# Kernel tuning notes

Hardware: AMD Instinct MI355X
Metric: run time of the kernel (lower is better)

The kernel has to match this reference:

```python
import jax, jax.numpy as jnp
import numpy as np

B, T, C = 2, 2048, 1024
H, DH = 16, 64          # n_heads = d_model // 64
WIN = 256               # sliding window size
K = 32                  # n_oscillators
DFF = 4096              # d_ff_hidden
NEG = -1e9


def setup_inputs() -> dict:
    key = jax.random.key(0)
    ks = jax.random.split(key, 16)
    sC = 1.0 / np.sqrt(C)
    sF = 1.0 / np.sqrt(DFF)
    sK = 1.0 / np.sqrt(K)
    return {
        "x": jax.random.normal(ks[0], (B, T, C), jnp.float32),
        "norm1_w": jnp.ones((C,), jnp.float32),
        "qkv_w": jax.random.normal(ks[1], (3 * C, C), jnp.float32) * sC,
        "qkv_b": jnp.zeros((3 * C,), jnp.float32),
        "proj_w": jax.random.normal(ks[2], (C, C), jnp.float32) * sC,
        "proj_b": jnp.zeros((C,), jnp.float32),
        "gate_w": jax.random.normal(ks[3], (1, C), jnp.float32) * 0.01,
        "gate_b": jnp.zeros((1,), jnp.float32),
        "trn_win": jax.random.normal(ks[4], (K, C), jnp.float32) * sC,
        "trn_wout": jax.random.normal(ks[5], (C, K), jnp.float32) * sK,
        "trn_gate_w": jax.random.normal(ks[6], (K, C), jnp.float32) * sC,
        "trn_gate_b": jnp.zeros((K,), jnp.float32),
        "trn_a_logit": jax.random.normal(ks[7], (K,), jnp.float32),
        "trn_theta": jax.random.uniform(ks[8], (K,), jnp.float32, 0.0, np.pi),
        "trn_res_scale": jnp.asarray(0.1, jnp.float32),
        "norm2_w": jnp.ones((C,), jnp.float32),
        "ffn_gate_w": jax.random.normal(ks[9], (DFF, C), jnp.float32) * sC,
        "ffn_up_w": jax.random.normal(ks[10], (DFF, C), jnp.float32) * sC,
        "ffn_down_w": jax.random.normal(ks[11], (C, DFF), jnp.float32) * sF,
    }


def _rms(z, w, eps=1e-6):
    return z * jax.lax.rsqrt(jnp.mean(z * z, axis=-1, keepdims=True) + eps) * w


def reference(x, norm1_w, qkv_w, qkv_b, proj_w, proj_b, gate_w, gate_b,
              trn_win, trn_wout, trn_gate_w, trn_gate_b, trn_a_logit,
              trn_theta, trn_res_scale, norm2_w, ffn_gate_w, ffn_up_w,
              ffn_down_w):
    h = _rms(x, norm1_w)

    # ---- windowed causal attention (dense mask, as in the original) ----
    qkv = h @ qkv_w.T + qkv_b                       # [B,T,3C]
    q, k, v = jnp.split(qkv, 3, axis=-1)
    heads = lambda t: t.reshape(B, T, H, DH).transpose(0, 2, 1, 3)  # [B,H,T,DH]
    q, k, v = heads(q), heads(k), heads(v)
    row = jnp.arange(T)[:, None]
    col = jnp.arange(T)[None, :]
    mask = jnp.where((col <= row) & (col >= row - WIN + 1), 0.0, NEG).astype(x.dtype)
    scores = jnp.einsum('bhqd,bhkd->bhqk', q, k) / jnp.sqrt(jnp.asarray(DH, x.dtype))
    attn = jax.nn.softmax(scores + mask, axis=-1)
    ao = jnp.einsum('bhqk,bhkd->bhqd', attn, v).transpose(0, 2, 1, 3).reshape(B, T, C)
    ao = ao @ proj_w.T + proj_b

    # ---- temporal resonance branch: K damped rotating oscillators ----
    u = h @ trn_win.T                               # [B,T,K] drive
    a = jax.nn.sigmoid(trn_a_logit)                 # amplitude in (0,1) (amplitude_max=1)
    ct, st = jnp.cos(trn_theta), jnp.sin(trn_theta)

    def step(carry, ut):
        sr, si = carry
        nsr = a * (ct * sr - st * si) + ut
        nsi = a * (st * sr + ct * si)
        return (nsr, nsi), nsr

    init = (jnp.zeros((B, K), x.dtype), jnp.zeros((B, K), x.dtype))
    _, ys = jax.lax.scan(step, init, u.transpose(1, 0, 2))  # ys: [T,B,K]
    y = ys.transpose(1, 0, 2)                                # [B,T,K]
    tg = jax.nn.sigmoid(h @ trn_gate_w.T + trn_gate_b)
    trn_out = ((tg * y) @ trn_wout.T) * trn_res_scale        # [B,T,C]

    # ---- sigmoid gate mix + residual ----
    g = jax.nn.sigmoid(h @ gate_w.T + gate_b)       # [B,T,1]
    x = x + g * ao + (1.0 - g) * trn_out

    # ---- SwiGLU FFN ----
    h2 = _rms(x, norm2_w)
    ffn = (jax.nn.silu(h2 @ ffn_gate_w.T) * (h2 @ ffn_up_w.T)) @ ffn_down_w.T
    return x + ffn
```

## Files before the change

kernel.cpp:

```cpp
#include <hip/hip_runtime.h>


typedef unsigned short u16;
typedef unsigned short u16x8 __attribute__((ext_vector_type(8)));
typedef __bf16 bf16x8 __attribute__((ext_vector_type(8)));
typedef float f32x4 __attribute__((ext_vector_type(4)));

#define DI static __device__ __forceinline__

DI u16 f2b(float f){
  union { float f; unsigned u; } v; v.f = f;
  unsigned r = v.u + 0x7FFFu + ((v.u >> 16) & 1u);
  return (u16)(r >> 16);
}
DI float b2f(u16 b){
  union { unsigned u; float f; } v; v.u = ((unsigned)b) << 16; return v.f;
}
DI u16x8 ld8(const u16* p){ return *(const u16x8*)p; }

DI f32x4 MFMA16(u16x8 a, u16x8 b, f32x4 c){
  return __builtin_amdgcn_mfma_f32_16x16x32_bf16(
      __builtin_bit_cast(bf16x8, a), __builtin_bit_cast(bf16x8, b), c, 0, 0, 0);
}

DI void async16(const void* g, void* l){
  void* gg = const_cast<void*>(g);
  __builtin_amdgcn_global_load_lds(
      (__attribute__((address_space(1))) void*)gg,
      (__attribute__((address_space(3))) void*)l, 16, 0, 0);
}

__global__ __launch_bounds__(256) void convert_w(
    const float* __restrict__ qkvw, const float* __restrict__ projw,
    const float* __restrict__ fgw, const float* __restrict__ fuw,
    const float* __restrict__ fdw, const float* __restrict__ twin,
    const float* __restrict__ tgw, const float* __restrict__ twout,
    u16* __restrict__ dst)
{
  size_t i = (size_t)blockIdx.x * 256 + threadIdx.x;
  if (i >= 4260352u) return;
  size_t e = i * 4;
  float4 v;
  if (e < 3145728u)        v = *(const float4*)(qkvw + e);
  else if (e < 4194304u)   v = *(const float4*)(projw + (e - 3145728u));
  else if (e < 12582912u){
    size_t i2 = e - 4194304u;
    int row = (int)(i2 >> 10), c = (int)(i2 & 1023);
    const float* src = (row & 1) ? fuw : fgw;
    v = *(const float4*)(src + (size_t)(row >> 1) * 1024 + c);
  }
  else if (e < 16777216u)  v = *(const float4*)(fdw + (e - 12582912u));
  else if (e < 16908288u){
    size_t i2 = e - 16777216u;
    int row = (int)(i2 >> 10), c = (int)(i2 & 1023);
    if (row < 32)      v = *(const float4*)(twin + row * 1024 + c);
    else if (row < 64) v = *(const float4*)(tgw + (row - 32) * 1024 + c);
    else               v = make_float4(0.f, 0.f, 0.f, 0.f);
  } else {
    v = *(const float4*)(twout + (e - 16908288u));
  }
  uint2 p;
  p.x = (unsigned)f2b(v.x) | ((unsigned)f2b(v.y) << 16);
  p.y = (unsigned)f2b(v.z) | ((unsigned)f2b(v.w) << 16);
  *(uint2*)(dst + e) = p;
}

__global__ __launch_bounds__(256) void zero_f32(float* __restrict__ p, int n4)
{
  int i = blockIdx.x * 256 + threadIdx.x;
  if (i < n4) ((float4*)p)[i] = make_float4(0.f, 0.f, 0.f, 0.f);
}

__global__ __launch_bounds__(256) void copy_f32(
    const float* __restrict__ src, float* __restrict__ dst)
{
  int i = blockIdx.x * 256 + threadIdx.x;
  ((float4*)dst)[i] = ((const float4*)src)[i];
}

__global__ __launch_bounds__(256) void rmsnorm_gate(
    const float* __restrict__ x, const float* __restrict__ w,
    const float* __restrict__ gw, const float* __restrict__ gb,
    u16* __restrict__ h, float* __restrict__ g)
{
  const int row = blockIdx.x, tid = threadIdx.x;
  const int wave = tid >> 6, lane = tid & 63;
  __shared__ float sb[8];
  float4 xv = ((const float4*)(x + (size_t)row * 1024))[tid];
  float ss = xv.x*xv.x + xv.y*xv.y + xv.z*xv.z + xv.w*xv.w;
#pragma unroll
  for (int m = 32; m; m >>= 1) ss += __shfl_xor(ss, m);
  if (lane == 0) sb[wave] = ss;
  __syncthreads();
  float rstd = rsqrtf((sb[0]+sb[1]+sb[2]+sb[3]) * (1.f/1024.f) + 1e-6f);
  float4 wv = ((const float4*)w)[tid];
  float h0 = xv.x*rstd*wv.x, h1 = xv.y*rstd*wv.y;
  float h2v = xv.z*rstd*wv.z, h3 = xv.w*rstd*wv.w;
  uint2 pk;
  pk.x = (unsigned)f2b(h0) | ((unsigned)f2b(h1) << 16);
  pk.y = (unsigned)f2b(h2v) | ((unsigned)f2b(h3) << 16);
  ((uint2*)(h + (size_t)row * 1024))[tid] = pk;
  float4 gv = ((const float4*)gw)[tid];
  float gd = h0*gv.x + h1*gv.y + h2v*gv.z + h3*gv.w;
#pragma unroll
  for (int m = 32; m; m >>= 1) gd += __shfl_xor(gd, m);
  if (lane == 0) sb[4 + wave] = gd;
  __syncthreads();
  if (tid == 0) g[row] = 1.f / (1.f + __expf(-(sb[4]+sb[5]+sb[6]+sb[7] + gb[0])));
}

__global__ __launch_bounds__(256) void rmsnorm_plain(
    const float* __restrict__ x, const float* __restrict__ w, u16* __restrict__ h)
{
  const int row = blockIdx.x, tid = threadIdx.x;
  const int wave = tid >> 6, lane = tid & 63;
  __shared__ float sb[4];
  float4 xv = ((const float4*)(x + (size_t)row * 1024))[tid];
  float ss = xv.x*xv.x + xv.y*xv.y + xv.z*xv.z + xv.w*xv.w;
#pragma unroll
  for (int m = 32; m; m >>= 1) ss += __shfl_xor(ss, m);
  if (lane == 0) sb[wave] = ss;
  __syncthreads();
  float rstd = rsqrtf((sb[0]+sb[1]+sb[2]+sb[3]) * (1.f/1024.f) + 1e-6f);
  float4 wv = ((const float4*)w)[tid];
  uint2 pk;
  pk.x = (unsigned)f2b(xv.x*rstd*wv.x) | ((unsigned)f2b(xv.y*rstd*wv.y) << 16);
  pk.y = (unsigned)f2b(xv.z*rstd*wv.z) | ((unsigned)f2b(xv.w*rstd*wv.w) << 16);
  ((uint2*)(h + (size_t)row * 1024))[tid] = pk;
}

template<int MODE>
__global__ __launch_bounds__(256) void gemm_bt(
    const u16* __restrict__ A, const u16* __restrict__ B,
    float* __restrict__ outF, float* __restrict__ outF2, u16* __restrict__ outB,
    const float* __restrict__ bias, const u16* __restrict__ aux16,
    const float* __restrict__ auxF, const float* __restrict__ auxG,
    int M, int N, int K)
{
  (void)M;
  __shared__ __align__(16) u16 sA[128 * 32];
  __shared__ __align__(16) u16 sB[128 * 32];
  const int tid = threadIdx.x;
  const int wave = tid >> 6, lane = tid & 63;
  const int lr = lane & 15, lq = lane >> 4;
  const int m0 = blockIdx.x * 128, n0 = blockIdx.y * 128;
  const int wm = (wave & 1) * 64, wn = (wave >> 1) * 64;
  const int ks = K / (int)gridDim.z;
  const int kbeg = (int)blockIdx.z * ks, kend = kbeg + ks;
  f32x4 acc[4][4] = {};
  const int srow = wave * 16 + (lane >> 2);
  const int scol = (lane & 3) * 8;
  const u16* gA = A + (size_t)(m0 + srow) * K + scol;
  const u16* gB = B + (size_t)(n0 + srow) * K + scol;
  u16* lA0 = &sA[(wave * 16) * 32];
  u16* lA1 = &sA[(64 + wave * 16) * 32];
  u16* lB0 = &sB[(wave * 16) * 32];
  u16* lB1 = &sB[(64 + wave * 16) * 32];
  const size_t K64 = (size_t)64 * K;

  for (int k0 = kbeg; k0 < kend; k0 += 32){
    async16(gA + k0,       lA0);
    async16(gA + K64 + k0, lA1);
    async16(gB + k0,       lB0);
    async16(gB + K64 + k0, lB1);
    __syncthreads();
    u16x8 af[4], bf[4];
#pragma unroll
    for (int i = 0; i < 4; i++) af[i] = ld8(&sA[(wm + i*16 + lr)*32 + lq*8]);
#pragma unroll
    for (int i = 0; i < 4; i++) bf[i] = ld8(&sB[(wn + i*16 + lr)*32 + lq*8]);
#pragma unroll
    for (int mi = 0; mi < 4; mi++)
#pragma unroll
      for (int ni = 0; ni < 4; ni++)
        acc[mi][ni] = MFMA16(af[mi], bf[ni], acc[mi][ni]);
    __syncthreads();
  }

  float scale6 = 0.f;
  if (MODE == 6) scale6 = auxF[0];

#pragma unroll
  for (int mi = 0; mi < 4; mi++){
    const int row = m0 + wm + mi*16 + lq*4;
#pragma unroll
    for (int ni = 0; ni < 4; ni++){
      const int col = n0 + wn + ni*16 + lr;
#pragma unroll
      for (int r = 0; r < 4; r++){
        const int rr = row + r;
        float v = acc[mi][ni][r];
        if (MODE == 0){
          outB[(size_t)rr * N + col] = f2b(v + bias[col]);
        } else if (MODE == 3){
          atomicAdd(&outF[(size_t)rr * N + col], v);
        } else if (MODE == 4){
          const size_t idx = (size_t)rr * N + col;
          float gg = auxG[rr];
          outF[idx] = auxF[idx] + gg * (v + bias[col]) + (1.f - gg) * b2f(aux16[idx]);
        } else if (MODE == 5){
          int bb = rr >> 11, tt = rr & 2047;
          if (col < 32) atomicAdd(&outF[((size_t)bb * 32 + col) * 2048 + tt], v);
          else if (col < 64) atomicAdd(&outF2[(size_t)rr * 32 + (col - 32)], v);
        } else if (MODE == 6){
          outB[(size_t)rr * N + col] = f2b(v * scale6);
        } else if (MODE == 7){
          float p = __shfl_xor(v, 1);
          float gval = (lr & 1) ? p : v;
          float uval = (lr & 1) ? v : p;
          float rv = gval / (1.f + __expf(-gval)) * uval;
          if (!(lr & 1))
            outB[(size_t)rr * (N >> 1) + (col >> 1)] = f2b(rv);
        }
      }
    }
  }
}

__global__ __launch_bounds__(256) void attn_win(
    const u16* __restrict__ qkv, u16* __restrict__ ao)
{
  const int blk = blockIdx.x;
  const int tile = blk & 31, hh = (blk >> 5) & 15, b = blk >> 9;
  const int t0 = tile * 64;
  const int tid = threadIdx.x, wave = tid >> 6, lane = tid & 63;
  const int lr = lane & 15, lq = lane >> 4;
  const int qt = t0 + wave * 16;
  __shared__ __align__(16) u16 sVt[64 * 40];
  __shared__ __align__(16) u16 sP[4][16 * 32];

  const u16* base = qkv + (size_t)b * 2048 * 3072 + hh * 64;
  const u16* qrow = base + (size_t)(qt + lr) * 3072 + lq * 8;
  u16x8 qf0 = ld8(qrow), qf1 = ld8(qrow + 32);
  const u16* kbase = base + 1024;
  const u16* vbase = base + 2048;

  f32x4 o0 = {0,0,0,0}, o1 = {0,0,0,0}, o2 = {0,0,0,0}, o3 = {0,0,0,0};
  float mrun[4] = {-1e30f, -1e30f, -1e30f, -1e30f};
  float lrun[4] = {0.f, 0.f, 0.f, 0.f};
  const float c1 = 0.125f * 1.44269504088896f;

  const int kb = (t0 >= 256) ? (t0 - 256) : 0;
  const int ntl = (t0 + 64 - kb) >> 5;
  for (int it = 0; it < ntl; ++it){
    const int kt = kb + it * 32;
    __syncthreads();
    if (tid < 128){
      const int key = tid & 31, dh = tid >> 5;
      const u16* gv = vbase + (size_t)(kt + key) * 3072 + dh * 16;
      u16x8 v0 = ld8(gv), v1 = ld8(gv + 8);
#pragma unroll
      for (int j = 0; j < 8; j++){
        sVt[(dh*16 + j)     * 40 + key] = v0[j];
        sVt[(dh*16 + 8 + j) * 40 + key] = v1[j];
      }
    }
    __syncthreads();
    const bool active = (kt < qt + 16) && (kt + 286 >= qt);
    if (!active) continue;

    f32x4 s0 = {0,0,0,0}, s1 = {0,0,0,0};
    {
      const u16* kr = kbase + (size_t)(kt + lr) * 3072 + lq * 8;
      u16x8 k00 = ld8(kr), k01 = ld8(kr + 32);
      const u16* kr1 = kr + (size_t)16 * 3072;
      u16x8 k10 = ld8(kr1), k11 = ld8(kr1 + 32);
      s0 = MFMA16(qf0, k00, s0); s0 = MFMA16(qf1, k01, s0);
      s1 = MFMA16(qf0, k10, s1); s1 = MFMA16(qf1, k11, s1);
    }
    float al[4];
#pragma unroll
    for (int r = 0; r < 4; r++){
      const int q = qt + lq * 4 + r;
      const int ca = kt + lr, cb = kt + 16 + lr;
      float a0 = (ca <= q && ca + 255 >= q) ? s0[r] : -1e30f;
      float a1 = (cb <= q && cb + 255 >= q) ? s1[r] : -1e30f;
      float mx = fmaxf(a0, a1);
      mx = fmaxf(mx, __shfl_xor(mx, 1));
      mx = fmaxf(mx, __shfl_xor(mx, 2));
      mx = fmaxf(mx, __shfl_xor(mx, 4));
      mx = fmaxf(mx, __shfl_xor(mx, 8));
      float mn = fmaxf(mrun[r], mx);
      al[r] = exp2f((mrun[r] - mn) * c1);
      mrun[r] = mn;
      float p0 = (a0 > -1e29f) ? exp2f((a0 - mn) * c1) : 0.f;
      float p1 = (a1 > -1e29f) ? exp2f((a1 - mn) * c1) : 0.f;
      float sm = p0 + p1;
      sm += __shfl_xor(sm, 1); sm += __shfl_xor(sm, 2);
      sm += __shfl_xor(sm, 4); sm += __shfl_xor(sm, 8);
      lrun[r] = lrun[r] * al[r] + sm;
      sP[wave][(lq*4 + r) * 32 + lr]      = f2b(p0);
      sP[wave][(lq*4 + r) * 32 + 16 + lr] = f2b(p1);
    }
#pragma unroll
    for (int r = 0; r < 4; r++){
      o0[r] *= al[r]; o1[r] *= al[r]; o2[r] *= al[r]; o3[r] *= al[r];
    }
    __builtin_amdgcn_s_waitcnt(0xc07f);
    u16x8 pf = ld8(&sP[wave][lr * 32 + lq * 8]);
    o0 = MFMA16(pf, ld8(&sVt[(lr)      * 40 + lq * 8]), o0);
    o1 = MFMA16(pf, ld8(&sVt[(16 + lr) * 40 + lq * 8]), o1);
    o2 = MFMA16(pf, ld8(&sVt[(32 + lr) * 40 + lq * 8]), o2);
    o3 = MFMA16(pf, ld8(&sVt[(48 + lr) * 40 + lq * 8]), o3);
  }

  u16* aor = ao + (size_t)(b * 2048 + qt + lq * 4) * 1024 + hh * 64 + lr;
#pragma unroll
  for (int r = 0; r < 4; r++){
    float inv = 1.f / lrun[r];
    u16* p = aor + (size_t)r * 1024;
    p[0]  = f2b(o0[r] * inv);
    p[16] = f2b(o1[r] * inv);
    p[32] = f2b(o2[r] * inv);
    p[48] = f2b(o3[r] * inv);
  }
}

__global__ __launch_bounds__(256) void scan_k(
    const float* __restrict__ u_t, const float* __restrict__ tgl,
    const float* __restrict__ tgb,
    const float* __restrict__ alog, const float* __restrict__ theta,
    u16* __restrict__ z)
{
  const int bk = blockIdx.x;
  const int b = bk >> 5, k = bk & 31;
  const int j = threadIdx.x;
  const float a = 1.f / (1.f + __expf(-alog[k]));
  const float th = theta[k];
  const float bk_bias = tgb[k];
  const float wr = a * __cosf(th), wi = a * __sinf(th);
  const float* ubp = u_t + ((size_t)b * 32 + k) * 2048 + j * 8;
  float4 ua = ((const float4*)ubp)[0];
  float4 ub4 = ((const float4*)ubp)[1];
  float ur[8] = {ua.x, ua.y, ua.z, ua.w, ub4.x, ub4.y, ub4.z, ub4.w};
  float sr = 0.f, si = 0.f;
#pragma unroll
  for (int i = 0; i < 8; i++){
    float nr = wr*sr - wi*si + ur[i];
    float ni = wi*sr + wr*si;
    sr = nr; si = ni;
  }
  float w2r = wr*wr - wi*wi, w2i = 2.f*wr*wi;
  float w4r = w2r*w2r - w2i*w2i, w4i = 2.f*w2r*w2i;
  float Ar = w4r*w4r - w4i*w4i, Ai = 2.f*w4r*w4i;
  __shared__ float4 sc[256];
  float4 cur; cur.x = Ar; cur.y = Ai; cur.z = sr; cur.w = si;
  sc[j] = cur;
  __syncthreads();
  for (int s = 1; s < 256; s <<= 1){
    float4 pv;
    const bool has = (j >= s);
    if (has) pv = sc[j - s];
    __syncthreads();
    if (has){
      float nar = cur.x*pv.x - cur.y*pv.y;
      float nai = cur.x*pv.y + cur.y*pv.x;
      float nbr = cur.x*pv.z - cur.y*pv.w + cur.z;
      float nbi = cur.x*pv.w + cur.y*pv.z + cur.w;
      cur.x = nar; cur.y = nai; cur.z = nbr; cur.w = nbi;
    }
    sc[j] = cur;
    __syncthreads();
  }
  float s_r = 0.f, s_i = 0.f;
  if (j > 0){ float4 pr = sc[j - 1]; s_r = pr.z; s_i = pr.w; }
  const float* tgp = tgl + ((size_t)b * 2048 + j * 8) * 32 + k;
  u16* zp = z + ((size_t)b * 2048 + j * 8) * 32 + k;
#pragma unroll
  for (int i = 0; i < 8; i++){
    float nr = wr*s_r - wi*s_i + ur[i];
    float ni = wi*s_r + wr*s_i;
    s_r = nr; s_i = ni;
    float tgv = 1.f / (1.f + __expf(-(tgp[(size_t)i * 32] + bk_bias)));
    zp[(size_t)i * 32] = f2b(s_r * tgv);
  }
}

extern "C" void kernel_launch(void* const* d_in, const int* in_sizes, int n_in,
                              void* d_out, int out_size, void* d_ws, size_t ws_size,
                              hipStream_t stream)
{
  (void)in_sizes; (void)n_in; (void)out_size; (void)ws_size;
  const float* x      = (const float*)d_in[0];
  const float* n1w    = (const float*)d_in[1];
  const float* qkvw   = (const float*)d_in[2];
  const float* qkvb   = (const float*)d_in[3];
  const float* projw  = (const float*)d_in[4];
  const float* projb  = (const float*)d_in[5];
  const float* gatew  = (const float*)d_in[6];
  const float* gateb  = (const float*)d_in[7];
  const float* twin   = (const float*)d_in[8];
  const float* twout  = (const float*)d_in[9];
  const float* tgw    = (const float*)d_in[10];
  const float* tgb    = (const float*)d_in[11];
  const float* talog  = (const float*)d_in[12];
  const float* ttheta = (const float*)d_in[13];
  const float* tscale = (const float*)d_in[14];
  const float* n2w    = (const float*)d_in[15];
  const float* fgw    = (const float*)d_in[16];
  const float* fuw    = (const float*)d_in[17];
  const float* fdw    = (const float*)d_in[18];
  float* out = (float*)d_out;

  char* wsb = (char*)d_ws;
  size_t off = 0;
  auto take = [&](size_t bytes) -> void* {
    void* r = wsb + off; off += (bytes + 255) & ~(size_t)255; return r;
  };
  u16*   wall = (u16*)take(17041408ull * 2);
  u16*   h    = (u16*)take(4194304ull * 2);
  u16*   h2   = (u16*)take(4194304ull * 2);
  u16*   trn  = (u16*)take(4194304ull * 2);
  float* g    = (float*)take(4096ull * 4);
  float* xmid = (float*)take(4194304ull * 4);
  float* uacc = (float*)take(262144ull * 4);
  float* tgl  = uacc + 131072;
  u16*   zz   = (u16*)take(131072ull * 2);
  u16*   regA = (u16*)take(4096ull * 4096 * 2);
  u16*   regB = (u16*)take(4096ull * 4096 * 2);

  u16* wq  = wall;
  u16* wp  = wall + 3145728;
  u16* wgu = wall + 4194304;
  u16* wd  = wall + 12582912;
  u16* wct = wall + 16777216;
  u16* wo  = wall + 16908288;
  u16* qkv = regA;
  u16* act = regA;
  u16* ao  = regB;

  convert_w<<<16642, 256, 0, stream>>>(qkvw, projw, fgw, fuw, fdw, twin, tgw, twout, wall);
  rmsnorm_gate<<<4096, 256, 0, stream>>>(x, n1w, gatew, gateb, h, g);
  zero_f32<<<256, 256, 0, stream>>>(uacc, 65536);
  gemm_bt<5><<<dim3(32, 1, 8), 256, 0, stream>>>(h, wct, uacc, tgl, nullptr, nullptr,
                                                 nullptr, nullptr, nullptr, 4096, 128, 1024);
  scan_k<<<64, 256, 0, stream>>>(uacc, tgl, tgb, talog, ttheta, zz);
  gemm_bt<6><<<dim3(32, 8), 256, 0, stream>>>(zz, wo, nullptr, nullptr, trn, nullptr,
                                              nullptr, tscale, nullptr, 4096, 1024, 32);
  gemm_bt<0><<<dim3(32, 24), 256, 0, stream>>>(h, wq, nullptr, nullptr, qkv, qkvb,
                                               nullptr, nullptr, nullptr, 4096, 3072, 1024);
  attn_win<<<1024, 256, 0, stream>>>(qkv, ao);
  gemm_bt<4><<<dim3(32, 8), 256, 0, stream>>>(ao, wp, xmid, nullptr, nullptr, projb,
                                              trn, x, g, 4096, 1024, 1024);
  rmsnorm_plain<<<4096, 256, 0, stream>>>(xmid, n2w, h2);
  gemm_bt<7><<<dim3(32, 64), 256, 0, stream>>>(h2, wgu, nullptr, nullptr, act, nullptr,
                                               nullptr, nullptr, nullptr, 4096, 8192, 1024);
  copy_f32<<<4096, 256, 0, stream>>>(xmid, out);
  gemm_bt<3><<<dim3(32, 8, 4), 256, 0, stream>>>(act, wd, out, nullptr, nullptr, nullptr,
                                                 nullptr, nullptr, nullptr, 4096, 1024, 4096);
}
```

Before: 496.8 us.

## Replace atomic split-K with partial buffers, fuse proj reduce with mix and norm

The proj GEMM becomes split-K=2 writing fp32 partials, reduced by a new kernel that also applies bias, gate mix, residual and RMSNorm2. This removes the separate rmsnorm pass and lets the proj GEMM use more blocks. The down GEMM drops from split-K 4 with atomics to split-K 2 with plain stores plus a reduce kernel that adds the residual, removing copy_f32 and the atomic traffic. The gate/up weights are re-interleaved in 16-row groups so the SwiGLU epilogue pairs accumulator tiles directly instead of shuffling lanes. The cost is extra fp32 partial-buffer traffic through memory.

```diff
diff --git a/kernel.cpp b/kernel.cpp
--- a/kernel.cpp
+++ b/kernel.cpp
@@ -46,8 +46,9 @@
   else if (e < 12582912u){
     size_t i2 = e - 4194304u;
     int row = (int)(i2 >> 10), c = (int)(i2 & 1023);
-    const float* src = (row & 1) ? fuw : fgw;
-    v = *(const float4*)(src + (size_t)(row >> 1) * 1024 + c);
+    int G = row >> 5, j = row & 31;
+    const float* src = (j < 16) ? fgw : fuw;
+    v = *(const float4*)(src + (size_t)(G * 16 + (j & 15)) * 1024 + c);
   }
   else if (e < 16777216u)  v = *(const float4*)(fdw + (e - 12582912u));
   else if (e < 16908288u){
@@ -69,13 +70,6 @@
 {
   int i = blockIdx.x * 256 + threadIdx.x;
   if (i < n4) ((float4*)p)[i] = make_float4(0.f, 0.f, 0.f, 0.f);
-}
-
-__global__ __launch_bounds__(256) void copy_f32(
-    const float* __restrict__ src, float* __restrict__ dst)
-{
-  int i = blockIdx.x * 256 + threadIdx.x;
-  ((float4*)dst)[i] = ((const float4*)src)[i];
 }
 
 __global__ __launch_bounds__(256) void rmsnorm_gate(
@@ -109,35 +103,64 @@
   if (tid == 0) g[row] = 1.f / (1.f + __expf(-(sb[4]+sb[5]+sb[6]+sb[7] + gb[0])));
 }
 
-__global__ __launch_bounds__(256) void rmsnorm_plain(
-    const float* __restrict__ x, const float* __restrict__ w, u16* __restrict__ h)
+__global__ __launch_bounds__(256) void reduce_mix_norm(
+    const float* __restrict__ part, const float* __restrict__ x,
+    const u16* __restrict__ trn, const float* __restrict__ g,
+    const float* __restrict__ pb, const float* __restrict__ n2w,
+    float* __restrict__ xmid, u16* __restrict__ h2)
 {
   const int row = blockIdx.x, tid = threadIdx.x;
   const int wave = tid >> 6, lane = tid & 63;
   __shared__ float sb[4];
-  float4 xv = ((const float4*)(x + (size_t)row * 1024))[tid];
-  float ss = xv.x*xv.x + xv.y*xv.y + xv.z*xv.z + xv.w*xv.w;
+  const size_t ro = (size_t)row * 1024;
+  float4 p0 = ((const float4*)(part + ro))[tid];
+  float4 p1 = ((const float4*)(part + 4194304 + ro))[tid];
+  float4 bb = ((const float4*)pb)[tid];
+  float4 xv = ((const float4*)(x + ro))[tid];
+  uint2 tz = ((const uint2*)(trn + ro))[tid];
+  float gg = g[row];
+  float t0 = b2f((u16)tz.x), t1 = b2f((u16)(tz.x >> 16));
+  float t2 = b2f((u16)tz.y), t3 = b2f((u16)(tz.y >> 16));
+  float m0 = xv.x + gg*(p0.x+p1.x+bb.x) + (1.f-gg)*t0;
+  float m1 = xv.y + gg*(p0.y+p1.y+bb.y) + (1.f-gg)*t1;
+  float m2 = xv.z + gg*(p0.z+p1.z+bb.z) + (1.f-gg)*t2;
+  float m3 = xv.w + gg*(p0.w+p1.w+bb.w) + (1.f-gg)*t3;
+  float4 mo; mo.x = m0; mo.y = m1; mo.z = m2; mo.w = m3;
+  ((float4*)(xmid + ro))[tid] = mo;
+  float ss = m0*m0 + m1*m1 + m2*m2 + m3*m3;
 #pragma unroll
   for (int m = 32; m; m >>= 1) ss += __shfl_xor(ss, m);
   if (lane == 0) sb[wave] = ss;
   __syncthreads();
   float rstd = rsqrtf((sb[0]+sb[1]+sb[2]+sb[3]) * (1.f/1024.f) + 1e-6f);
-  float4 wv = ((const float4*)w)[tid];
+  float4 wv = ((const float4*)n2w)[tid];
   uint2 pk;
-  pk.x = (unsigned)f2b(xv.x*rstd*wv.x) | ((unsigned)f2b(xv.y*rstd*wv.y) << 16);
-  pk.y = (unsigned)f2b(xv.z*rstd*wv.z) | ((unsigned)f2b(xv.w*rstd*wv.w) << 16);
-  ((uint2*)(h + (size_t)row * 1024))[tid] = pk;
+  pk.x = (unsigned)f2b(m0*rstd*wv.x) | ((unsigned)f2b(m1*rstd*wv.y) << 16);
+  pk.y = (unsigned)f2b(m2*rstd*wv.z) | ((unsigned)f2b(m3*rstd*wv.w) << 16);
+  ((uint2*)(h2 + ro))[tid] = pk;
+}
+
+__global__ __launch_bounds__(256) void reduce_down(
+    const float* __restrict__ part, const float* __restrict__ xmid,
+    float* __restrict__ out)
+{
+  size_t i = (size_t)blockIdx.x * 256 + threadIdx.x;
+  float4 p0 = ((const float4*)part)[i];
+  float4 p1 = ((const float4*)(part + 4194304))[i];
+  float4 xv = ((const float4*)xmid)[i];
+  float4 o;
+  o.x = xv.x + p0.x + p1.x; o.y = xv.y + p0.y + p1.y;
+  o.z = xv.z + p0.z + p1.z; o.w = xv.w + p0.w + p1.w;
+  ((float4*)out)[i] = o;
 }
 
 template<int MODE>
 __global__ __launch_bounds__(256) void gemm_bt(
     const u16* __restrict__ A, const u16* __restrict__ B,
     float* __restrict__ outF, float* __restrict__ outF2, u16* __restrict__ outB,
-    const float* __restrict__ bias, const u16* __restrict__ aux16,
-    const float* __restrict__ auxF, const float* __restrict__ auxG,
+    const float* __restrict__ bias, const float* __restrict__ auxF,
     int M, int N, int K)
 {
-  (void)M;
   __shared__ __align__(16) u16 sA[128 * 32];
   __shared__ __align__(16) u16 sB[128 * 32];
   const int tid = threadIdx.x;
@@ -177,6 +200,25 @@
     __syncthreads();
   }
 
+  if (MODE == 7){
+    const int cb = ((n0 + wn) >> 1) + lr;
+#pragma unroll
+    for (int mi = 0; mi < 4; mi++){
+      const int row = m0 + wm + mi*16 + lq*4;
+#pragma unroll
+      for (int p = 0; p < 2; p++){
+        const int col = cb + p*16;
+#pragma unroll
+        for (int r = 0; r < 4; r++){
+          float gv = acc[mi][2*p][r], uv = acc[mi][2*p+1][r];
+          float rv = gv / (1.f + __expf(-gv)) * uv;
+          outB[(size_t)(row + r) * (N >> 1) + col] = f2b(rv);
+        }
+      }
+    }
+    return;
+  }
+
   float scale6 = 0.f;
   if (MODE == 6) scale6 = auxF[0];
 
@@ -192,25 +234,14 @@
         float v = acc[mi][ni][r];
         if (MODE == 0){
           outB[(size_t)rr * N + col] = f2b(v + bias[col]);
-        } else if (MODE == 3){
-          atomicAdd(&outF[(size_t)rr * N + col], v);
-        } else if (MODE == 4){
-          const size_t idx = (size_t)rr * N + col;
-          float gg = auxG[rr];
-          outF[idx] = auxF[idx] + gg * (v + bias[col]) + (1.f - gg) * b2f(aux16[idx]);
         } else if (MODE == 5){
           int bb = rr >> 11, tt = rr & 2047;
           if (col < 32) atomicAdd(&outF[((size_t)bb * 32 + col) * 2048 + tt], v);
           else if (col < 64) atomicAdd(&outF2[(size_t)rr * 32 + (col - 32)], v);
         } else if (MODE == 6){
           outB[(size_t)rr * N + col] = f2b(v * scale6);
-        } else if (MODE == 7){
-          float p = __shfl_xor(v, 1);
-          float gval = (lr & 1) ? p : v;
-          float uval = (lr & 1) ? v : p;
-          float rv = gval / (1.f + __expf(-gval)) * uval;
-          if (!(lr & 1))
-            outB[(size_t)rr * (N >> 1) + (col >> 1)] = f2b(rv);
+        } else if (MODE == 8){
+          outF[(size_t)blockIdx.z * (size_t)M + (size_t)rr * N + col] = v;
         }
       }
     }
@@ -425,27 +456,29 @@
   u16* wd  = wall + 12582912;
   u16* wct = wall + 16777216;
   u16* wo  = wall + 16908288;
-  u16* qkv = regA;
-  u16* act = regA;
-  u16* ao  = regB;
+  u16*   qkv   = regA;
+  float* pproj = (float*)regA;
+  u16*   act   = regA;
+  u16*   ao    = regB;
+  float* pdown = (float*)regB;
 
   convert_w<<<16642, 256, 0, stream>>>(qkvw, projw, fgw, fuw, fdw, twin, tgw, twout, wall);
   rmsnorm_gate<<<4096, 256, 0, stream>>>(x, n1w, gatew, gateb, h, g);
   zero_f32<<<256, 256, 0, stream>>>(uacc, 65536);
   gemm_bt<5><<<dim3(32, 1, 8), 256, 0, stream>>>(h, wct, uacc, tgl, nullptr, nullptr,
-                                                 nullptr, nullptr, nullptr, 4096, 128, 1024);
+                                                 nullptr, 0, 128, 1024);
   scan_k<<<64, 256, 0, stream>>>(uacc, tgl, tgb, talog, ttheta, zz);
   gemm_bt<6><<<dim3(32, 8), 256, 0, stream>>>(zz, wo, nullptr, nullptr, trn, nullptr,
-                                              nullptr, tscale, nullptr, 4096, 1024, 32);
+                                              tscale, 0, 1024, 32);
   gemm_bt<0><<<dim3(32, 24), 256, 0, stream>>>(h, wq, nullptr, nullptr, qkv, qkvb,
-                                               nullptr, nullptr, nullptr, 4096, 3072, 1024);
+                                               nullptr, 0, 3072, 1024);
   attn_win<<<1024, 256, 0, stream>>>(qkv, ao);
-  gemm_bt<4><<<dim3(32, 8), 256, 0, stream>>>(ao, wp, xmid, nullptr, nullptr, projb,
-                                              trn, x, g, 4096, 1024, 1024);
-  rmsnorm_plain<<<4096, 256, 0, stream>>>(xmid, n2w, h2);
+  gemm_bt<8><<<dim3(32, 8, 2), 256, 0, stream>>>(ao, wp, pproj, nullptr, nullptr, nullptr,
+                                                 nullptr, 4194304, 1024, 1024);
+  reduce_mix_norm<<<4096, 256, 0, stream>>>(pproj, x, trn, g, projb, n2w, xmid, h2);
   gemm_bt<7><<<dim3(32, 64), 256, 0, stream>>>(h2, wgu, nullptr, nullptr, act, nullptr,
-                                               nullptr, nullptr, nullptr, 4096, 8192, 1024);
-  copy_f32<<<4096, 256, 0, stream>>>(xmid, out);
-  gemm_bt<3><<<dim3(32, 8, 4), 256, 0, stream>>>(act, wd, out, nullptr, nullptr, nullptr,
-                                                 nullptr, nullptr, nullptr, 4096, 1024, 4096);
-}
+                                               nullptr, 0, 8192, 1024);
+  gemm_bt<8><<<dim3(32, 8, 2), 256, 0, stream>>>(act, wd, pdown, nullptr, nullptr, nullptr,
+                                                 nullptr, 4194304, 1024, 4096);
+  reduce_down<<<4096, 256, 0, stream>>>(pdown, xmid, out);
+}
```

New measurement: 449.6 us. -9.5%, faster.
